# Kernel tuning notes

Hardware: AMD Instinct MI355X
Metric: run time of the kernel (lower is better)

Reference implementation:

```python
import jax, jax.numpy as jnp
import numpy as np

N, E = 50000, 800000
F_IN, F_EMB1, F_EMB2, F_HID, F_OUT = 128, 512, 128, 1024, 64


def _linear_params(k, fan_in, fan_out):
    s = 1.0 / np.sqrt(fan_in)
    kw, kb = jax.random.split(k)
    W = jax.random.uniform(kw, (fan_in, fan_out), jnp.float32, -s, s)
    b = jax.random.uniform(kb, (fan_out,), jnp.float32, -s, s)
    return W, b


def setup_inputs() -> dict:
    key = jax.random.key(0)
    ks = jax.random.split(key, 8)
    x = jax.random.normal(ks[0], (N, F_IN), jnp.float32)
    src = jax.random.randint(ks[1], (E,), 0, N)
    dst = jax.random.randint(ks[2], (E,), 0, N)
    edge_index = jnp.stack([src, dst])  # [2, E]
    edge_weight = jax.random.uniform(ks[3], (E,), jnp.float32)  # positive weights
    W1, b1 = _linear_params(ks[4], F_IN, F_EMB1)
    W2, b2 = _linear_params(ks[5], F_EMB1, F_EMB2)
    W3, b3 = _linear_params(ks[6], F_EMB2, F_HID)
    W4, b4 = _linear_params(ks[7], F_HID, F_OUT)
    return dict(x=x, edge_index=edge_index, edge_weight=edge_weight,
                W1=W1, b1=b1, W2=W2, b2=b2, W3=W3, b3=b3, W4=W4, b4=b4)


def gcn_conv(x, src, dst, w, W, b):
    """PyG GCNConv: transform, then sym-normalized weighted aggregation with self-loops.
    out = D^{-1/2} (A_w + I) D^{-1/2} (x W) + b,  deg = scatter(w @ dst) + 1."""
    n = x.shape[0]
    h = x @ W  # [N, F_out]
    deg = jax.ops.segment_sum(w, dst, num_segments=n) + 1.0  # +1 for self-loop weight
    dinv = jax.lax.rsqrt(deg)
    norm = dinv[src] * w * dinv[dst]  # [E]
    agg = jax.ops.segment_sum(norm[:, None] * h[src], dst, num_segments=n)
    agg = agg + h / deg[:, None]  # self-loop: dinv[i]*1*dinv[i] * h[i]
    return agg + b


def reference(x, edge_index, edge_weight, W1, b1, W2, b2, W3, b3, W4, b4):
    src, dst = edge_index[0], edge_index[1]
    h = jax.nn.relu(gcn_conv(x, src, dst, edge_weight, W1, b1))
    # graph_normalization=False -> identity; dropout is identity in eval mode
    h = jax.nn.relu(gcn_conv(h, src, dst, edge_weight, W2, b2))
    h = jax.nn.relu(h @ W3 + b3)
    out = jax.nn.relu(h @ W4 + b4)
    return out
```

## Files before the change

kernel.cpp:

```cpp
#include <hip/hip_runtime.h>


#define ELLW 64

typedef short bf16x8 __attribute__((ext_vector_type(8)));
typedef float f32x4 __attribute__((ext_vector_type(4)));

__device__ __forceinline__ unsigned short f2b(float f) {
    unsigned u = __builtin_bit_cast(unsigned, f);
    unsigned r = (u + 0x7FFFu + ((u >> 16) & 1u)) >> 16;
    return (unsigned short)r;
}
__device__ __forceinline__ float b2f(unsigned short u) {
    return __builtin_bit_cast(float, (unsigned)u << 16);
}

__global__ void k_zero_int(int* p, int n) {
    int i = blockIdx.x * 256 + threadIdx.x;
    if (i < n) p[i] = 0;
}

__global__ void k_fill_ell(const int* __restrict__ src, const int* __restrict__ dst,
                           const float* __restrict__ w, int* __restrict__ cnt,
                           int* __restrict__ s_src, float* __restrict__ s_w, int E) {
    int e = blockIdx.x * 256 + threadIdx.x;
    if (e >= E) return;
    int d = dst[e];
    int slot = atomicAdd(&cnt[d], 1);
    if (slot < ELLW) {
        size_t idx = (size_t)d * ELLW + slot;
        s_src[idx] = src[e];
        s_w[idx] = w[e];
    }
}

__global__ __launch_bounds__(256) void k_deg(const float* __restrict__ s_w,
                                             const int* __restrict__ cnt,
                                             float* __restrict__ dinv, int Nn) {
    int node = blockIdx.x * 4 + (threadIdx.x >> 6);
    if (node >= Nn) return;
    int lane = threadIdx.x & 63;
    int c = min(cnt[node], ELLW);
    float s = (lane < c) ? s_w[(size_t)node * ELLW + lane] : 0.0f;
    #pragma unroll
    for (int d = 32; d > 0; d >>= 1) s += __shfl_down(s, d);
    if (lane == 0) dinv[node] = rsqrtf(1.0f + s);
}

__global__ void k_f2b4(const float* __restrict__ in, unsigned short* __restrict__ out, int n4) {
    int i = blockIdx.x * 256 + threadIdx.x;
    if (i >= n4) return;
    float4 v = ((const float4*)in)[i];
    ushort4 o;
    o.x = f2b(v.x); o.y = f2b(v.y); o.z = f2b(v.z); o.w = f2b(v.w);
    ((ushort4*)out)[i] = o;
}

__global__ void k_wt_all(const float* __restrict__ W1, const float* __restrict__ W2,
                         const float* __restrict__ W3, const float* __restrict__ W4,
                         unsigned short* __restrict__ W1t, unsigned short* __restrict__ W2t,
                         unsigned short* __restrict__ W3t, unsigned short* __restrict__ W4t) {
    int i = blockIdx.x * 256 + threadIdx.x;
    if (i < 65536) {
        int k = i >> 9, n = i & 511;
        W1t[n * 128 + k] = f2b(W1[i]);
    } else if (i < 131072) {
        int j = i - 65536; int k = j >> 7, n = j & 127;
        W2t[n * 512 + k] = f2b(W2[j]);
    } else if (i < 262144) {
        int j = i - 131072; int k = j >> 10, n = j & 1023;
        W3t[n * 128 + k] = f2b(W3[j]);
    } else {
        int j = i - 262144; int k = j >> 6, n = j & 63;
        W4t[n * 1024 + k] = f2b(W4[j]);
    }
}

template <bool FIRST, bool BIAS_RELU>
__global__ __launch_bounds__(256) void k_gather(
    const unsigned short* __restrict__ Xb, const int* __restrict__ s_src,
    float* __restrict__ s_w, const int* __restrict__ cnt,
    const float* __restrict__ dinv, const float* __restrict__ bias,
    unsigned short* __restrict__ outb, int Nn) {
    int node = blockIdx.x * 4 + (threadIdx.x >> 6);
    if (node >= Nn) return;
    int lane = threadIdx.x & 63;
    float di = dinv[node];
    float dii = di * di;
    ushort2 sv = ((const ushort2*)(Xb + (size_t)node * 128))[lane];
    float ax = b2f(sv.x) * dii, ay = b2f(sv.y) * dii;

    int c = min(cnt[node], ELLW);
    size_t base = (size_t)node * ELLW;
    int sreg = 0;
    float nv = 0.0f;
    if (lane < c) {
        sreg = s_src[base + lane];
        float wv = s_w[base + lane];
        if (FIRST) {
            nv = dinv[sreg] * wv * di;
            s_w[base + lane] = nv;
        } else {
            nv = wv;
        }
    }

    int j = 0;
    for (; j + 4 <= c; j += 4) {
        int s0 = __shfl(sreg, j),     s1 = __shfl(sreg, j + 1);
        int s2 = __shfl(sreg, j + 2), s3 = __shfl(sreg, j + 3);
        float n0 = __shfl(nv, j),     n1 = __shfl(nv, j + 1);
        float n2 = __shfl(nv, j + 2), n3 = __shfl(nv, j + 3);
        ushort2 r0 = ((const ushort2*)(Xb + (size_t)s0 * 128))[lane];
        ushort2 r1 = ((const ushort2*)(Xb + (size_t)s1 * 128))[lane];
        ushort2 r2 = ((const ushort2*)(Xb + (size_t)s2 * 128))[lane];
        ushort2 r3 = ((const ushort2*)(Xb + (size_t)s3 * 128))[lane];
        ax += n0 * b2f(r0.x) + n1 * b2f(r1.x) + n2 * b2f(r2.x) + n3 * b2f(r3.x);
        ay += n0 * b2f(r0.y) + n1 * b2f(r1.y) + n2 * b2f(r2.y) + n3 * b2f(r3.y);
    }
    for (; j < c; ++j) {
        int sj = __shfl(sreg, j);
        float nj = __shfl(nv, j);
        ushort2 r = ((const ushort2*)(Xb + (size_t)sj * 128))[lane];
        ax += nj * b2f(r.x);
        ay += nj * b2f(r.y);
    }

    if (BIAS_RELU) {
        float2 bv = ((const float2*)bias)[lane];
        ax = fmaxf(ax + bv.x, 0.0f);
        ay = fmaxf(ay + bv.y, 0.0f);
    }
    ushort2 o; o.x = f2b(ax); o.y = f2b(ay);
    ((ushort2*)(outb + (size_t)node * 128))[lane] = o;
}

template <int H, int OUTW, bool HAS_BO, bool OUT_BF16>
__global__ __launch_bounds__(256) void k_mlp(
    const unsigned short* __restrict__ A, const unsigned short* __restrict__ Wht,
    const unsigned short* __restrict__ Wot, const float* __restrict__ bh,
    const float* __restrict__ bo, void* __restrict__ out, int M) {
    constexpr int HC = H / 64;
    constexpr int NJ = OUTW / 16;
    constexpr int OW4 = OUTW / 32;
    __shared__ __align__(16) unsigned short Whs[64 * 128];
    __shared__ __align__(16) unsigned short Ps[64 * 64];
    __shared__ __align__(16) unsigned short Wos[OUTW * 64];
    const int tid = threadIdx.x, wave = tid >> 6, lane = tid & 63;
    const int lm = lane & 15, quad = lane >> 4;
    const int bm0 = blockIdx.x * 64;

    bf16x8 af[4];
    {
        int gr = bm0 + wave * 16 + lm;
        #pragma unroll
        for (int kb = 0; kb < 4; ++kb) af[kb] = bf16x8{0, 0, 0, 0, 0, 0, 0, 0};
        if (gr < M) {
            #pragma unroll
            for (int kb = 0; kb < 4; ++kb)
                af[kb] = *(const bf16x8*)(A + (size_t)gr * 128 + kb * 32 + quad * 8);
        }
    }

    #pragma unroll
    for (int u = 0; u < 4; ++u) {
        int idx = tid + u * 256; int r = idx >> 4, g = idx & 15;
        *(int4*)&Whs[r * 128 + ((g ^ (r & 15)) * 8)] =
            *(const int4*)(Wht + (size_t)r * 128 + g * 8);
    }
    #pragma unroll
    for (int u = 0; u < OW4; ++u) {
        int idx = tid + u * 256; int r = idx >> 3, g = idx & 7;
        *(int4*)&Wos[r * 64 + ((g ^ (r & 7)) * 8)] =
            *(const int4*)(Wot + (size_t)r * H + g * 8);
    }
    __syncthreads();

    f32x4 oacc[NJ] = {};
    for (int c = 0; c < HC; ++c) {
        f32x4 hacc[4] = {};
        #pragma unroll
        for (int kb = 0; kb < 4; ++kb) {
            bf16x8 bfr[4];
            #pragma unroll
            for (int j = 0; j < 4; ++j) {
                int r = j * 16 + lm, g = kb * 4 + quad;
                bfr[j] = *(const bf16x8*)&Whs[r * 128 + ((g ^ (r & 15)) * 8)];
            }
            #pragma unroll
            for (int j = 0; j < 4; ++j)
                hacc[j] = __builtin_amdgcn_mfma_f32_16x16x32_bf16(af[kb], bfr[j], hacc[j], 0, 0, 0);
        }

        #pragma unroll
        for (int j = 0; j < 4; ++j) {
            int col = j * 16 + lm;
            float bv = bh[c * 64 + col];
            #pragma unroll
            for (int r4 = 0; r4 < 4; ++r4) {
                int row = wave * 16 + quad * 4 + r4;
                float o = fmaxf(hacc[j][r4] + bv, 0.0f);
                Ps[row * 64 + (((col >> 3) ^ (row & 7)) * 8) + (col & 7)] = f2b(o);
            }
        }

        #pragma unroll
        for (int kb = 0; kb < 2; ++kb) {
            bf16x8 pf;
            {
                int r = wave * 16 + lm, g = kb * 4 + quad;
                pf = *(const bf16x8*)&Ps[r * 64 + ((g ^ (r & 7)) * 8)];
            }
            #pragma unroll
            for (int j = 0; j < NJ; ++j) {
                int r = j * 16 + lm, g = kb * 4 + quad;
                bf16x8 wf = *(const bf16x8*)&Wos[r * 64 + ((g ^ (r & 7)) * 8)];
                oacc[j] = __builtin_amdgcn_mfma_f32_16x16x32_bf16(pf, wf, oacc[j], 0, 0, 0);
            }
        }

        if (c + 1 < HC) {
            __syncthreads();
            #pragma unroll
            for (int u = 0; u < 4; ++u) {
                int idx = tid + u * 256; int r = idx >> 4, g = idx & 15;
                *(int4*)&Whs[r * 128 + ((g ^ (r & 15)) * 8)] =
                    *(const int4*)(Wht + (size_t)((c + 1) * 64 + r) * 128 + g * 8);
            }
            #pragma unroll
            for (int u = 0; u < OW4; ++u) {
                int idx = tid + u * 256; int r = idx >> 3, g = idx & 7;
                *(int4*)&Wos[r * 64 + ((g ^ (r & 7)) * 8)] =
                    *(const int4*)(Wot + (size_t)r * H + (c + 1) * 64 + g * 8);
            }
            __syncthreads();
        }
    }

    #pragma unroll
    for (int j = 0; j < NJ; ++j) {
        int col = j * 16 + lm;
        float bv = HAS_BO ? bo[col] : 0.0f;
        #pragma unroll
        for (int r4 = 0; r4 < 4; ++r4) {
            int m = bm0 + wave * 16 + quad * 4 + r4;
            if (m < M) {
                float o = oacc[j][r4];
                if (HAS_BO) o = fmaxf(o + bv, 0.0f);
                if (OUT_BF16)
                    ((unsigned short*)out)[(size_t)m * OUTW + col] = f2b(o);
                else
                    ((float*)out)[(size_t)m * OUTW + col] = o;
            }
        }
    }
}

static inline int cdiv(long a, long b) { return (int)((a + b - 1) / b); }

extern "C" void kernel_launch(void* const* d_in, const int* in_sizes, int n_in,
                              void* d_out, int out_size, void* d_ws, size_t ws_size,
                              hipStream_t stream) {
    const float* x  = (const float*)d_in[0];
    const int*   ei = (const int*)d_in[1];
    const float* ew = (const float*)d_in[2];
    const float* W1 = (const float*)d_in[3];
    const float* b1 = (const float*)d_in[4];
    const float* W2 = (const float*)d_in[5];
    const float* b2 = (const float*)d_in[6];
    const float* W3 = (const float*)d_in[7];
    const float* b3 = (const float*)d_in[8];
    const float* W4 = (const float*)d_in[9];
    const float* b4 = (const float*)d_in[10];
    const int Nn = in_sizes[0] / 128;
    const int E  = in_sizes[1] / 2;
    const int* src = ei;
    const int* dst = ei + E;

    char* ws = (char*)d_ws;
    size_t off_b = 0;
    auto alloc = [&](size_t bytes) -> void* {
        void* p = ws + off_b;
        off_b += (bytes + 255) & ~(size_t)255;
        return p;
    };
    float*          dinv  = (float*)alloc((size_t)Nn * 4);
    int*            cnt   = (int*)alloc((size_t)Nn * 4);
    int*            s_src = (int*)alloc((size_t)Nn * ELLW * 4);
    float*          s_w   = (float*)alloc((size_t)Nn * ELLW * 4);
    unsigned short* W1t   = (unsigned short*)alloc(512 * 128 * 2);
    unsigned short* W2t   = (unsigned short*)alloc(128 * 512 * 2);
    unsigned short* W3t   = (unsigned short*)alloc(1024 * 128 * 2);
    unsigned short* W4t   = (unsigned short*)alloc(64 * 1024 * 2);
    unsigned short* xb    = (unsigned short*)alloc((size_t)Nn * 128 * 2);
    unsigned short* t2b   = (unsigned short*)alloc((size_t)Nn * 128 * 2);
    unsigned short* actb  = (unsigned short*)alloc((size_t)Nn * 128 * 2);
    float*          out   = (float*)d_out;

    k_zero_int<<<cdiv(Nn, 256), 256, 0, stream>>>(cnt, Nn);
    k_fill_ell<<<cdiv(E, 256), 256, 0, stream>>>(src, dst, ew, cnt, s_src, s_w, E);
    k_deg<<<cdiv(Nn, 4), 256, 0, stream>>>(s_w, cnt, dinv, Nn);

    k_wt_all<<<1280, 256, 0, stream>>>(W1, W2, W3, W4, W1t, W2t, W3t, W4t);
    k_f2b4<<<cdiv((size_t)Nn * 32, 256), 256, 0, stream>>>(x, xb, Nn * 32);

    k_gather<true, false><<<cdiv(Nn, 4), 256, 0, stream>>>(
        xb, s_src, s_w, cnt, dinv, nullptr, actb, Nn);
    k_mlp<512, 128, false, true><<<cdiv(Nn, 64), 256, 0, stream>>>(
        actb, W1t, W2t, b1, nullptr, t2b, Nn);

    k_gather<false, true><<<cdiv(Nn, 4), 256, 0, stream>>>(
        t2b, s_src, s_w, cnt, dinv, b2, actb, Nn);

    k_mlp<1024, 64, true, false><<<cdiv(Nn, 64), 256, 0, stream>>>(
        actb, W3t, W4t, b3, b4, out, Nn);
}
```

Measured before the change: 311.9 us.

## Merge setup kernels, interleave edge src/weight, unroll gather loop by eight

The count-zeroing, weight transpose/convert and x-to-bf16 kernels are combined into one launch partitioned by block index, removing two kernel launches. ELL src and weight arrays are interleaved into one int2 record so each edge slot needs a single 8-byte load and store. The gather inner loop is unrolled from four to eight neighbours to keep more row loads in flight. The risks are a hardcoded grid layout (196 blocks for cnt, 7726 total) that assumes N=50000, and higher register use in the gather.

```diff
diff --git a/kernel.cpp b/kernel.cpp
--- a/kernel.cpp
+++ b/kernel.cpp
@@ -15,73 +15,72 @@
     return __builtin_bit_cast(float, (unsigned)u << 16);
 }
 
-__global__ void k_zero_int(int* p, int n) {
-    int i = blockIdx.x * 256 + threadIdx.x;
-    if (i < n) p[i] = 0;
+__global__ void k_setup(const float* __restrict__ x,
+                        const float* __restrict__ W1, const float* __restrict__ W2,
+                        const float* __restrict__ W3, const float* __restrict__ W4,
+                        unsigned short* __restrict__ W1t, unsigned short* __restrict__ W2t,
+                        unsigned short* __restrict__ W3t, unsigned short* __restrict__ W4t,
+                        unsigned short* __restrict__ xb, int* __restrict__ cnt, int Nn) {
+    int b = blockIdx.x;
+    if (b < 196) {
+        int i = b * 256 + threadIdx.x;
+        if (i < Nn) cnt[i] = 0;
+    } else if (b < 1476) {
+        int i = (b - 196) * 256 + threadIdx.x;
+        if (i < 65536) {
+            int k = i >> 9, n = i & 511;
+            W1t[n * 128 + k] = f2b(W1[i]);
+        } else if (i < 131072) {
+            int j = i - 65536; int k = j >> 7, n = j & 127;
+            W2t[n * 512 + k] = f2b(W2[j]);
+        } else if (i < 262144) {
+            int j = i - 131072; int k = j >> 10, n = j & 1023;
+            W3t[n * 128 + k] = f2b(W3[j]);
+        } else {
+            int j = i - 262144; int k = j >> 6, n = j & 63;
+            W4t[n * 1024 + k] = f2b(W4[j]);
+        }
+    } else {
+        int i = (b - 1476) * 256 + threadIdx.x;
+        if (i < Nn * 32) {
+            float4 v = ((const float4*)x)[i];
+            ushort4 o;
+            o.x = f2b(v.x); o.y = f2b(v.y); o.z = f2b(v.z); o.w = f2b(v.w);
+            ((ushort4*)xb)[i] = o;
+        }
+    }
 }
 
 __global__ void k_fill_ell(const int* __restrict__ src, const int* __restrict__ dst,
                            const float* __restrict__ w, int* __restrict__ cnt,
-                           int* __restrict__ s_src, float* __restrict__ s_w, int E) {
+                           int2* __restrict__ s_edge, int E) {
     int e = blockIdx.x * 256 + threadIdx.x;
     if (e >= E) return;
     int d = dst[e];
+    int2 rec = make_int2(src[e], __builtin_bit_cast(int, w[e]));
     int slot = atomicAdd(&cnt[d], 1);
-    if (slot < ELLW) {
-        size_t idx = (size_t)d * ELLW + slot;
-        s_src[idx] = src[e];
-        s_w[idx] = w[e];
-    }
-}
-
-__global__ __launch_bounds__(256) void k_deg(const float* __restrict__ s_w,
+    if (slot < ELLW) s_edge[(size_t)d * ELLW + slot] = rec;
+}
+
+__global__ __launch_bounds__(256) void k_deg(const int2* __restrict__ s_edge,
                                              const int* __restrict__ cnt,
                                              float* __restrict__ dinv, int Nn) {
     int node = blockIdx.x * 4 + (threadIdx.x >> 6);
     if (node >= Nn) return;
     int lane = threadIdx.x & 63;
     int c = min(cnt[node], ELLW);
-    float s = (lane < c) ? s_w[(size_t)node * ELLW + lane] : 0.0f;
+    float s = 0.0f;
+    if (lane < c) s = __builtin_bit_cast(float, s_edge[(size_t)node * ELLW + lane].y);
     #pragma unroll
     for (int d = 32; d > 0; d >>= 1) s += __shfl_down(s, d);
     if (lane == 0) dinv[node] = rsqrtf(1.0f + s);
 }
 
-__global__ void k_f2b4(const float* __restrict__ in, unsigned short* __restrict__ out, int n4) {
-    int i = blockIdx.x * 256 + threadIdx.x;
-    if (i >= n4) return;
-    float4 v = ((const float4*)in)[i];
-    ushort4 o;
-    o.x = f2b(v.x); o.y = f2b(v.y); o.z = f2b(v.z); o.w = f2b(v.w);
-    ((ushort4*)out)[i] = o;
-}
-
-__global__ void k_wt_all(const float* __restrict__ W1, const float* __restrict__ W2,
-                         const float* __restrict__ W3, const float* __restrict__ W4,
-                         unsigned short* __restrict__ W1t, unsigned short* __restrict__ W2t,
-                         unsigned short* __restrict__ W3t, unsigned short* __restrict__ W4t) {
-    int i = blockIdx.x * 256 + threadIdx.x;
-    if (i < 65536) {
-        int k = i >> 9, n = i & 511;
-        W1t[n * 128 + k] = f2b(W1[i]);
-    } else if (i < 131072) {
-        int j = i - 65536; int k = j >> 7, n = j & 127;
-        W2t[n * 512 + k] = f2b(W2[j]);
-    } else if (i < 262144) {
-        int j = i - 131072; int k = j >> 10, n = j & 1023;
-        W3t[n * 128 + k] = f2b(W3[j]);
-    } else {
-        int j = i - 262144; int k = j >> 6, n = j & 63;
-        W4t[n * 1024 + k] = f2b(W4[j]);
-    }
-}
-
 template <bool FIRST, bool BIAS_RELU>
 __global__ __launch_bounds__(256) void k_gather(
-    const unsigned short* __restrict__ Xb, const int* __restrict__ s_src,
-    float* __restrict__ s_w, const int* __restrict__ cnt,
-    const float* __restrict__ dinv, const float* __restrict__ bias,
-    unsigned short* __restrict__ outb, int Nn) {
+    const unsigned short* __restrict__ Xb, int2* __restrict__ s_edge,
+    const int* __restrict__ cnt, const float* __restrict__ dinv,
+    const float* __restrict__ bias, unsigned short* __restrict__ outb, int Nn) {
     int node = blockIdx.x * 4 + (threadIdx.x >> 6);
     if (node >= Nn) return;
     int lane = threadIdx.x & 63;
@@ -95,28 +94,39 @@
     int sreg = 0;
     float nv = 0.0f;
     if (lane < c) {
-        sreg = s_src[base + lane];
-        float wv = s_w[base + lane];
+        int2 rec = s_edge[base + lane];
+        sreg = rec.x;
         if (FIRST) {
+            float wv = __builtin_bit_cast(float, rec.y);
             nv = dinv[sreg] * wv * di;
-            s_w[base + lane] = nv;
+            ((int*)s_edge)[2 * (base + lane) + 1] = __builtin_bit_cast(int, nv);
         } else {
-            nv = wv;
+            nv = __builtin_bit_cast(float, rec.y);
         }
     }
 
     int j = 0;
-    for (; j + 4 <= c; j += 4) {
+    for (; j + 8 <= c; j += 8) {
         int s0 = __shfl(sreg, j),     s1 = __shfl(sreg, j + 1);
         int s2 = __shfl(sreg, j + 2), s3 = __shfl(sreg, j + 3);
+        int s4 = __shfl(sreg, j + 4), s5 = __shfl(sreg, j + 5);
+        int s6 = __shfl(sreg, j + 6), s7 = __shfl(sreg, j + 7);
         float n0 = __shfl(nv, j),     n1 = __shfl(nv, j + 1);
         float n2 = __shfl(nv, j + 2), n3 = __shfl(nv, j + 3);
+        float n4 = __shfl(nv, j + 4), n5 = __shfl(nv, j + 5);
+        float n6 = __shfl(nv, j + 6), n7 = __shfl(nv, j + 7);
         ushort2 r0 = ((const ushort2*)(Xb + (size_t)s0 * 128))[lane];
         ushort2 r1 = ((const ushort2*)(Xb + (size_t)s1 * 128))[lane];
         ushort2 r2 = ((const ushort2*)(Xb + (size_t)s2 * 128))[lane];
         ushort2 r3 = ((const ushort2*)(Xb + (size_t)s3 * 128))[lane];
+        ushort2 r4 = ((const ushort2*)(Xb + (size_t)s4 * 128))[lane];
+        ushort2 r5 = ((const ushort2*)(Xb + (size_t)s5 * 128))[lane];
+        ushort2 r6 = ((const ushort2*)(Xb + (size_t)s6 * 128))[lane];
+        ushort2 r7 = ((const ushort2*)(Xb + (size_t)s7 * 128))[lane];
         ax += n0 * b2f(r0.x) + n1 * b2f(r1.x) + n2 * b2f(r2.x) + n3 * b2f(r3.x);
         ay += n0 * b2f(r0.y) + n1 * b2f(r1.y) + n2 * b2f(r2.y) + n3 * b2f(r3.y);
+        ax += n4 * b2f(r4.x) + n5 * b2f(r5.x) + n6 * b2f(r6.x) + n7 * b2f(r7.x);
+        ay += n4 * b2f(r4.y) + n5 * b2f(r5.y) + n6 * b2f(r6.y) + n7 * b2f(r7.y);
     }
     for (; j < c; ++j) {
         int sj = __shfl(sreg, j);
@@ -284,33 +294,29 @@
         off_b += (bytes + 255) & ~(size_t)255;
         return p;
     };
-    float*          dinv  = (float*)alloc((size_t)Nn * 4);
-    int*            cnt   = (int*)alloc((size_t)Nn * 4);
-    int*            s_src = (int*)alloc((size_t)Nn * ELLW * 4);
-    float*          s_w   = (float*)alloc((size_t)Nn * ELLW * 4);
-    unsigned short* W1t   = (unsigned short*)alloc(512 * 128 * 2);
-    unsigned short* W2t   = (unsigned short*)alloc(128 * 512 * 2);
-    unsigned short* W3t   = (unsigned short*)alloc(1024 * 128 * 2);
-    unsigned short* W4t   = (unsigned short*)alloc(64 * 1024 * 2);
-    unsigned short* xb    = (unsigned short*)alloc((size_t)Nn * 128 * 2);
-    unsigned short* t2b   = (unsigned short*)alloc((size_t)Nn * 128 * 2);
-    unsigned short* actb  = (unsigned short*)alloc((size_t)Nn * 128 * 2);
-    float*          out   = (float*)d_out;
-
-    k_zero_int<<<cdiv(Nn, 256), 256, 0, stream>>>(cnt, Nn);
-    k_fill_ell<<<cdiv(E, 256), 256, 0, stream>>>(src, dst, ew, cnt, s_src, s_w, E);
-    k_deg<<<cdiv(Nn, 4), 256, 0, stream>>>(s_w, cnt, dinv, Nn);
-
-    k_wt_all<<<1280, 256, 0, stream>>>(W1, W2, W3, W4, W1t, W2t, W3t, W4t);
-    k_f2b4<<<cdiv((size_t)Nn * 32, 256), 256, 0, stream>>>(x, xb, Nn * 32);
+    float*          dinv   = (float*)alloc((size_t)Nn * 4);
+    int*            cnt    = (int*)alloc((size_t)Nn * 4);
+    int2*           s_edge = (int2*)alloc((size_t)Nn * ELLW * 8);
+    unsigned short* W1t    = (unsigned short*)alloc(512 * 128 * 2);
+    unsigned short* W2t    = (unsigned short*)alloc(128 * 512 * 2);
+    unsigned short* W3t    = (unsigned short*)alloc(1024 * 128 * 2);
+    unsigned short* W4t    = (unsigned short*)alloc(64 * 1024 * 2);
+    unsigned short* xb     = (unsigned short*)alloc((size_t)Nn * 128 * 2);
+    unsigned short* t2b    = (unsigned short*)alloc((size_t)Nn * 128 * 2);
+    unsigned short* actb   = (unsigned short*)alloc((size_t)Nn * 128 * 2);
+    float*          out    = (float*)d_out;
+
+    k_setup<<<7726, 256, 0, stream>>>(x, W1, W2, W3, W4, W1t, W2t, W3t, W4t, xb, cnt, Nn);
+    k_fill_ell<<<cdiv(E, 256), 256, 0, stream>>>(src, dst, ew, cnt, s_edge, E);
+    k_deg<<<cdiv(Nn, 4), 256, 0, stream>>>(s_edge, cnt, dinv, Nn);
 
     k_gather<true, false><<<cdiv(Nn, 4), 256, 0, stream>>>(
-        xb, s_src, s_w, cnt, dinv, nullptr, actb, Nn);
+        xb, s_edge, cnt, dinv, nullptr, actb, Nn);
     k_mlp<512, 128, false, true><<<cdiv(Nn, 64), 256, 0, stream>>>(
         actb, W1t, W2t, b1, nullptr, t2b, Nn);
 
     k_gather<false, true><<<cdiv(Nn, 4), 256, 0, stream>>>(
-        t2b, s_src, s_w, cnt, dinv, b2, actb, Nn);
+        t2b, s_edge, cnt, dinv, b2, actb, Nn);
 
     k_mlp<1024, 64, true, false><<<cdiv(Nn, 64), 256, 0, stream>>>(
         actb, W3t, W4t, b3, b4, out, Nn);
```

After: 306.4 us. About the same (-1.8%).
